# Optimization experiments

Hardware: AMD Instinct MI355X
Metric: run time of the kernel (lower is better)

## Reference

```python
import jax, jax.numpy as jnp
import numpy as np

N_NODES = 50000
N_EDGES = 200000
D = 384
R = 2  # num_relations


def setup_inputs() -> dict:
    key = jax.random.key(0)
    ks = jax.random.split(key, 16)
    inp = {
        "embeddings": jax.random.normal(ks[0], (N_NODES, D), dtype=jnp.float32),
        "edge_index": jax.random.randint(ks[1], (2, N_EDGES), 0, N_NODES, dtype=jnp.int64),
        "edge_type": jax.random.randint(ks[2], (N_EDGES,), 0, R, dtype=jnp.int64),
    }
    # RGCNConv params for 3 layers: per-relation weight, root weight, bias
    s = 1.0 / np.sqrt(D)
    for i, kk in zip((1, 2, 3), range(3)):
        inp[f"W{i}"] = jax.random.uniform(ks[3 + 3 * kk], (R, D, D), dtype=jnp.float32, minval=-s, maxval=s)
        inp[f"root{i}"] = jax.random.uniform(ks[4 + 3 * kk], (D, D), dtype=jnp.float32, minval=-s, maxval=s)
        inp[f"bias{i}"] = jnp.zeros((D,), dtype=jnp.float32)
    return inp


def _rgcn_conv(x, src, dst, edge_type, W, root, bias):
    # PyG RGCNConv with aggr='mean': for each relation, mean-aggregate neighbor
    # features over edges of that relation, then apply relation weight; plus
    # root transform and bias. We transform-then-aggregate (equivalent, linear).
    out = x @ root + bias
    for r in range(R):
        xr = x @ W[r]                                   # [N, D]
        mask = (edge_type == r).astype(x.dtype)         # [E]
        msg = xr[src] * mask[:, None]                   # [E, D] gather
        s = jax.ops.segment_sum(msg, dst, num_segments=N_NODES)    # [N, D]
        cnt = jax.ops.segment_sum(mask, dst, num_segments=N_NODES)  # [N]
        out = out + s / jnp.maximum(cnt, 1.0)[:, None]  # mean (0 if no edges)
    return out


def reference(embeddings, edge_index, edge_type, W1, root1, bias1, W2, root2, bias2, W3, root3, bias3):
    src, dst = edge_index[0], edge_index[1]
    x = jax.nn.relu(_rgcn_conv(embeddings, src, dst, edge_type, W1, root1, bias1))
    # dropout is identity in eval mode
    x = jax.nn.relu(_rgcn_conv(x, src, dst, edge_type, W2, root2, bias2))
    x = _rgcn_conv(x, src, dst, edge_type, W3, root3, bias3)
    return x
```

## Files before the change

### kernel.cpp

```cpp
#include <hip/hip_runtime.h>
#include <hip/hip_bf16.h>


#define D 384
#define KC 1152
#define BM 128
#define BN 128
#define BK 32
#define NKT (KC / BK)
#define NTN (D / BN)

typedef __attribute__((ext_vector_type(8))) short short8;
typedef __attribute__((ext_vector_type(4))) float floatx4;
typedef unsigned int uint;
typedef unsigned short ushort;

#define BAR() asm volatile("s_barrier" ::: "memory")
#define WAIT_VM4() asm volatile("s_waitcnt vmcnt(4)" ::: "memory")
#define WAIT_VM0() asm volatile("s_waitcnt vmcnt(0)" ::: "memory")

__device__ __forceinline__ void load_lds16(const void* g, void* l) {
    __builtin_amdgcn_global_load_lds(
        (const __attribute__((address_space(1))) void*)g,
        (__attribute__((address_space(3))) void*)l, 16, 0, 0);
}

__device__ __forceinline__ ushort f2bf(float x) {
    __hip_bfloat16 h = __float2bfloat16(x);
    return *reinterpret_cast<ushort*>(&h);
}

__device__ __forceinline__ uint pack2(float a, float b) {
    return (uint)f2bf(a) | ((uint)f2bf(b) << 16);
}

__device__ __forceinline__ void stage_rows(const ushort* __restrict__ g,
                                           size_t stride, int koff,
                                           ushort* l, int grow0, int rmax,
                                           int tid)
{
#pragma unroll
    for (int j = 0; j < 2; ++j) {
        const int ch = j * 256 + tid;
        const int row = ch >> 2;
        const int cs = ch & 3;
        const int gc = cs ^ ((row >> 1) & 3);
        const int gr = min(grow0 + row, rmax);
        load_lds16(g + (size_t)gr * stride + koff + gc * 8, l + (size_t)ch * 8);
    }
}

__global__ __launch_bounds__(256, 3) void gemm_fused(
    const ushort* __restrict__ X, const ushort* __restrict__ AG,
    const ushort* __restrict__ BT, const float* __restrict__ bias,
    ushort* __restrict__ Xn, float* __restrict__ outf,
    int M, int nwg, int relu)
{
    __shared__ alignas(16) ushort As[3][BM * BK];
    __shared__ alignas(16) ushort Bs[3][BN * BK];

    const int o = blockIdx.x;
    const int xcd = o & 7, lid = o >> 3;
    const int q = nwg >> 3, r = nwg & 7;
    const int wg = (xcd < r ? xcd * (q + 1) : r * (q + 1) + (xcd - r) * q) + lid;
    const int bnt = wg % NTN, bmt = wg / NTN;
    const int bm = bmt * BM, bn = bnt * BN;

    const int tid = threadIdx.x;
    const int wave = tid >> 6, lane = tid & 63;
    const int wm = wave >> 1;
    const int wn = wave & 1;
    const int l15 = lane & 15, k8 = lane >> 4;

    floatx4 acc[4][4] = {};

    auto stage_a = [&](int kt, ushort* dst) {
        if (kt < 12) stage_rows(X, 384, kt * BK, dst, bm, M - 1, tid);
        else         stage_rows(AG, 768, (kt - 12) * BK, dst, bm, M - 1, tid);
    };

    stage_a(0, As[0]);
    stage_rows(BT, KC, 0, Bs[0], bn, D - 1, tid);
    stage_a(1, As[1]);
    stage_rows(BT, KC, BK, Bs[1], bn, D - 1, tid);
    WAIT_VM4();
    BAR();

    for (int j = 0; j < NKT; ++j) {
        const ushort* Ab = As[j % 3];
        const ushort* Bb = Bs[j % 3];

        short8 af[4], bf[4];
#pragma unroll
        for (int nf = 0; nf < 4; ++nf) {
            const int rr = wn * 64 + nf * 16 + l15;
            af[nf] = *(const short8*)(Bb + rr * BK + ((k8 ^ ((rr >> 1) & 3)) << 3));
        }
#pragma unroll
        for (int mf = 0; mf < 4; ++mf) {
            const int rr = wm * 64 + mf * 16 + l15;
            bf[mf] = *(const short8*)(Ab + rr * BK + ((k8 ^ ((rr >> 1) & 3)) << 3));
        }

        const int js = j + 2;
        if (js < NKT) {
            stage_a(js, As[js % 3]);
            stage_rows(BT, KC, js * BK, Bs[js % 3], bn, D - 1, tid);
        }

        __builtin_amdgcn_s_setprio(1);
#pragma unroll
        for (int nf = 0; nf < 4; ++nf)
#pragma unroll
            for (int mf = 0; mf < 4; ++mf)
                acc[nf][mf] = __builtin_amdgcn_mfma_f32_16x16x32_bf16(
                    af[nf], bf[mf], acc[nf][mf], 0, 0, 0);
        __builtin_amdgcn_s_setprio(0);

        if (j <= NKT - 3)      { WAIT_VM4(); }
        else if (j == NKT - 2) { WAIT_VM0(); }
        BAR();
    }

    const int node0 = bm + wm * 64 + l15;
    const int colg = bn + wn * 64 + k8 * 4;
    float4 bv[4];
#pragma unroll
    for (int nf = 0; nf < 4; ++nf)
        bv[nf] = *(const float4*)(bias + colg + nf * 16);

#pragma unroll
    for (int mf = 0; mf < 4; ++mf) {
        const int node = node0 + mf * 16;
        if (node < M) {
            float v[4][4];
#pragma unroll
            for (int nf = 0; nf < 4; ++nf) {
                v[nf][0] = acc[nf][mf][0] + bv[nf].x;
                v[nf][1] = acc[nf][mf][1] + bv[nf].y;
                v[nf][2] = acc[nf][mf][2] + bv[nf].z;
                v[nf][3] = acc[nf][mf][3] + bv[nf].w;
                if (relu) {
#pragma unroll
                    for (int t = 0; t < 4; ++t) v[nf][t] = fmaxf(v[nf][t], 0.f);
                }
            }
            if (Xn) {
                uint2* rowp = (uint2*)(Xn + (size_t)node * D + colg);
#pragma unroll
                for (int nf = 0; nf < 4; ++nf) {
                    uint2 o2;
                    o2.x = pack2(v[nf][0], v[nf][1]);
                    o2.y = pack2(v[nf][2], v[nf][3]);
                    rowp[nf * 4] = o2;
                }
            } else {
                float4* rowp = (float4*)(outf + (size_t)node * D + colg);
#pragma unroll
                for (int nf = 0; nf < 4; ++nf)
                    rowp[nf * 4] = make_float4(v[nf][0], v[nf][1],
                                               v[nf][2], v[nf][3]);
            }
        }
    }
}


__global__ __launch_bounds__(256) void count_edges(
    const int* __restrict__ dst, const int* __restrict__ et,
    int* __restrict__ cntI, int E, int M)
{
    const int e = blockIdx.x * blockDim.x + threadIdx.x;
    if (e < E) atomicAdd(&cntI[(size_t)et[e] * M + dst[e]], 1);
}

__global__ __launch_bounds__(256) void finalize_cnt(
    const int* __restrict__ cntI, float* __restrict__ invc, int n)
{
    const int i = blockIdx.x * blockDim.x + threadIdx.x;
    if (i < n) invc[i] = 1.0f / (float)max(cntI[i], 1);
}

__global__ __launch_bounds__(1024) void scan_local(
    const int* __restrict__ hist, int* __restrict__ offs,
    int* __restrict__ bsums, int n)
{
    __shared__ int tmp[1024];
    const int tid = threadIdx.x;
    const int i = blockIdx.x * 1024 + tid;
    const int v = (i < n) ? hist[i] : 0;
    tmp[tid] = v;
    __syncthreads();
#pragma unroll
    for (int off = 1; off < 1024; off <<= 1) {
        const int add = (tid >= off) ? tmp[tid - off] : 0;
        __syncthreads();
        tmp[tid] += add;
        __syncthreads();
    }
    if (i < n) offs[i] = tmp[tid] - v;
    if (tid == 1023) bsums[blockIdx.x] = tmp[1023];
}

__global__ __launch_bounds__(1024) void scan_bsums(
    int* __restrict__ bsums, int* __restrict__ total_out, int nb)
{
    __shared__ int tmp[1024];
    const int tid = threadIdx.x;
    const int v = (tid < nb) ? bsums[tid] : 0;
    tmp[tid] = v;
    __syncthreads();
#pragma unroll
    for (int off = 1; off < 1024; off <<= 1) {
        const int add = (tid >= off) ? tmp[tid - off] : 0;
        __syncthreads();
        tmp[tid] += add;
        __syncthreads();
    }
    if (tid < nb) bsums[tid] = tmp[tid] - v;
    if (tid == 1023) *total_out = tmp[1023];
}

__global__ __launch_bounds__(1024) void scan_add(
    int* __restrict__ offs, const int* __restrict__ bsums, int n)
{
    const int i = blockIdx.x * 1024 + threadIdx.x;
    if (i < n) offs[i] += bsums[blockIdx.x];
}

__global__ __launch_bounds__(256) void fill_sorted(
    const int* __restrict__ src, const int* __restrict__ dst,
    const int* __restrict__ et, const int* __restrict__ offs,
    int* __restrict__ cursor, int* __restrict__ sorted, int E, int M)
{
    const int e = blockIdx.x * blockDim.x + threadIdx.x;
    if (e < E) {
        const int key = et[e] * M + dst[e];
        const int pos = offs[key] + atomicAdd(&cursor[key], 1);
        sorted[pos] = src[e];
    }
}

__global__ __launch_bounds__(256) void build_bt(
    const float* __restrict__ root1, const float* __restrict__ W1,
    const float* __restrict__ root2, const float* __restrict__ W2,
    const float* __restrict__ root3, const float* __restrict__ W3,
    ushort* __restrict__ BT)
{
    __shared__ float tile[32][33];
    const int l = blockIdx.z;
    const float* root = (l == 0) ? root1 : (l == 1) ? root2 : root3;
    const float* W    = (l == 0) ? W1    : (l == 1) ? W2    : W3;
    const int k0 = blockIdx.x * 32;
    const int n0 = blockIdx.y * 32;
    const int tx = threadIdx.x & 31;
    const int ty = threadIdx.x >> 5;
    const float* srcm;
    int koff;
    if (k0 < D)          { srcm = root;      koff = 0; }
    else if (k0 < 2 * D) { srcm = W;         koff = D; }
    else                 { srcm = W + D * D; koff = 2 * D; }
#pragma unroll
    for (int i = 0; i < 4; ++i) {
        const int k = k0 - koff + ty + i * 8;
        tile[ty + i * 8][tx] = srcm[(size_t)k * D + n0 + tx];
    }
    __syncthreads();
    ushort* dst = BT + (size_t)l * D * KC;
#pragma unroll
    for (int i = 0; i < 4; ++i) {
        const int nn = n0 + ty + i * 8;
        const int kk = k0 + tx;
        dst[(size_t)nn * KC + kk] = f2bf(tile[tx][ty + i * 8]);
    }
}

__global__ __launch_bounds__(256) void cast_f32_to_bf16(
    const float* __restrict__ x, ushort* __restrict__ y, int n4)
{
    const int i = blockIdx.x * blockDim.x + threadIdx.x;
    if (i < n4) {
        const float4 v = ((const float4*)x)[i];
        uint2 o;
        o.x = pack2(v.x, v.y);
        o.y = pack2(v.z, v.w);
        ((uint2*)y)[i] = o;
    }
}

__global__ __launch_bounds__(256) void aggregate_rel(
    const ushort* __restrict__ X, const int* __restrict__ sorted,
    const int* __restrict__ offs, const float* __restrict__ invc,
    ushort* __restrict__ AG, int M)
{
    const int wave = threadIdx.x >> 6;
    const int lane = threadIdx.x & 63;
    const int d = blockIdx.x * 4 + wave;
    if (d >= M) return;

#pragma unroll
    for (int r = 0; r < 2; ++r) {
        const int key = r * M + d;
        const int beg = offs[key], end = offs[key + 1];
        float g[6] = {0.f, 0.f, 0.f, 0.f, 0.f, 0.f};
        for (int i = beg; i < end; ++i) {
            const int s = sorted[i];
            const uint* tp = (const uint*)(X + (size_t)s * D);
#pragma unroll
            for (int p = 0; p < 3; ++p) {
                const uint b = tp[lane + 64 * p];
                g[2 * p]     += __uint_as_float(b << 16);
                g[2 * p + 1] += __uint_as_float(b & 0xffff0000u);
            }
        }
        const float ic = invc[key];
        uint* op = (uint*)(AG + (size_t)d * (2 * D) + r * D);
#pragma unroll
        for (int p = 0; p < 3; ++p)
            op[lane + 64 * p] = pack2(ic * g[2 * p], ic * g[2 * p + 1]);
    }
}

extern "C" void kernel_launch(void* const* d_in, const int* in_sizes, int n_in,
                              void* d_out, int out_size, void* d_ws, size_t ws_size,
                              hipStream_t stream)
{
    const float* emb   = (const float*)d_in[0];
    const int*   eidx  = (const int*)d_in[1];
    const int*   et    = (const int*)d_in[2];
    const float* W1    = (const float*)d_in[3];
    const float* root1 = (const float*)d_in[4];
    const float* bias1 = (const float*)d_in[5];
    const float* W2    = (const float*)d_in[6];
    const float* root2 = (const float*)d_in[7];
    const float* bias2 = (const float*)d_in[8];
    const float* W3    = (const float*)d_in[9];
    const float* root3 = (const float*)d_in[10];
    const float* bias3 = (const float*)d_in[11];

    float* out = (float*)d_out;
    const int M = in_sizes[0] / D;
    const int E = in_sizes[1] / 2;
    const int* src  = eidx;
    const int* dstv = eidx + E;

    const int n = 2 * M;
    const int nb = (n + 1023) / 1024;

    char* w = (char*)d_ws;
    ushort* Xa  = (ushort*)w;         w += (size_t)M * D * 2;
    ushort* Xb2 = (ushort*)w;         w += (size_t)M * D * 2;
    ushort* AG  = (ushort*)w;         w += (size_t)M * 2 * D * 2;
    ushort* BT  = (ushort*)w;         w += (size_t)3 * D * KC * 2;
    float* invcnt = (float*)w;        w += (size_t)n * 4;
    int* cntI = (int*)w;              w += (size_t)n * 4;
    int* offs = (int*)w;              w += ((size_t)n + 1) * 4;
    int* sorted = (int*)w;            w += (size_t)E * 4;
    int* bsums = (int*)w;

    hipMemsetAsync(cntI, 0, (size_t)n * sizeof(int), stream);
    count_edges<<<(E + 255) / 256, 256, 0, stream>>>(dstv, et, cntI, E, M);
    finalize_cnt<<<(n + 255) / 256, 256, 0, stream>>>(cntI, invcnt, n);
    scan_local<<<nb, 1024, 0, stream>>>(cntI, offs, bsums, n);
    scan_bsums<<<1, 1024, 0, stream>>>(bsums, offs + n, nb);
    scan_add<<<nb, 1024, 0, stream>>>(offs, bsums, n);
    hipMemsetAsync(cntI, 0, (size_t)n * sizeof(int), stream);
    fill_sorted<<<(E + 255) / 256, 256, 0, stream>>>(src, dstv, et, offs, cntI, sorted, E, M);

    build_bt<<<dim3(KC / 32, D / 32, 3), 256, 0, stream>>>(root1, W1, root2, W2, root3, W3, BT);
    cast_f32_to_bf16<<<(M * D / 4 + 255) / 256, 256, 0, stream>>>(emb, Xa, M * D / 4);

    const int Mtiles = (M + BM - 1) / BM;
    const int nwg = Mtiles * NTN;
    const int agg_blocks = (M + 3) / 4;

    aggregate_rel<<<agg_blocks, 256, 0, stream>>>(Xa, sorted, offs, invcnt, AG, M);
    gemm_fused<<<nwg, 256, 0, stream>>>(Xa, AG, BT, bias1, Xb2, nullptr, M, nwg, 1);
    aggregate_rel<<<agg_blocks, 256, 0, stream>>>(Xb2, sorted, offs, invcnt, AG, M);
    gemm_fused<<<nwg, 256, 0, stream>>>(Xb2, AG, BT + (size_t)D * KC, bias2, Xa, nullptr, M, nwg, 1);
    aggregate_rel<<<agg_blocks, 256, 0, stream>>>(Xa, sorted, offs, invcnt, AG, M);
    gemm_fused<<<nwg, 256, 0, stream>>>(Xa, AG, BT + (size_t)2 * D * KC, bias3, nullptr, out, M, nwg, 0);
}
```

Measured before the change: 487.1 us.

## Load weight tiles directly to registers and stage A via registers with double-buffered LDS

```diff
diff --git a/kernel.cpp b/kernel.cpp
--- a/kernel.cpp
+++ b/kernel.cpp
@@ -15,15 +15,7 @@
 typedef unsigned int uint;
 typedef unsigned short ushort;
 
-#define BAR() asm volatile("s_barrier" ::: "memory")
-#define WAIT_VM4() asm volatile("s_waitcnt vmcnt(4)" ::: "memory")
-#define WAIT_VM0() asm volatile("s_waitcnt vmcnt(0)" ::: "memory")
-
-__device__ __forceinline__ void load_lds16(const void* g, void* l) {
-    __builtin_amdgcn_global_load_lds(
-        (const __attribute__((address_space(1))) void*)g,
-        (__attribute__((address_space(3))) void*)l, 16, 0, 0);
-}
+#define LGKM0_BAR() asm volatile("s_waitcnt lgkmcnt(0)\n\ts_barrier" ::: "memory")
 
 __device__ __forceinline__ ushort f2bf(float x) {
     __hip_bfloat16 h = __float2bfloat16(x);
@@ -32,22 +24,6 @@
 
 __device__ __forceinline__ uint pack2(float a, float b) {
     return (uint)f2bf(a) | ((uint)f2bf(b) << 16);
-}
-
-__device__ __forceinline__ void stage_rows(const ushort* __restrict__ g,
-                                           size_t stride, int koff,
-                                           ushort* l, int grow0, int rmax,
-                                           int tid)
-{
-#pragma unroll
-    for (int j = 0; j < 2; ++j) {
-        const int ch = j * 256 + tid;
-        const int row = ch >> 2;
-        const int cs = ch & 3;
-        const int gc = cs ^ ((row >> 1) & 3);
-        const int gr = min(grow0 + row, rmax);
-        load_lds16(g + (size_t)gr * stride + koff + gc * 8, l + (size_t)ch * 8);
-    }
 }
 
 __global__ __launch_bounds__(256, 3) void gemm_fused(
@@ -56,8 +32,8 @@
     ushort* __restrict__ Xn, float* __restrict__ outf,
     int M, int nwg, int relu)
 {
-    __shared__ alignas(16) ushort As[3][BM * BK];
-    __shared__ alignas(16) ushort Bs[3][BN * BK];
+    __shared__ alignas(16) ushort As0[BM * BK];
+    __shared__ alignas(16) ushort As1[BM * BK];
 
     const int o = blockIdx.x;
     const int xcd = o & 7, lid = o >> 3;
@@ -74,52 +50,86 @@
 
     floatx4 acc[4][4] = {};
 
-    auto stage_a = [&](int kt, ushort* dst) {
-        if (kt < 12) stage_rows(X, 384, kt * BK, dst, bm, M - 1, tid);
-        else         stage_rows(AG, 768, (kt - 12) * BK, dst, bm, M - 1, tid);
+    int agr[2], agc[2];
+#pragma unroll
+    for (int jj = 0; jj < 2; ++jj) {
+        const int ch = jj * 256 + tid;
+        const int row = ch >> 2, cs = ch & 3;
+        agc[jj] = cs ^ ((row >> 1) & 3);
+        agr[jj] = min(bm + row, M - 1);
+    }
+
+    auto aglob = [&](int kt, short8* ar) {
+#pragma unroll
+        for (int jj = 0; jj < 2; ++jj) {
+            const ushort* p = (kt < 12)
+                ? X + (size_t)agr[jj] * 384 + kt * BK
+                : AG + (size_t)agr[jj] * 768 + (kt - 12) * BK;
+            ar[jj] = *(const short8*)(p + agc[jj] * 8);
+        }
     };
-
-    stage_a(0, As[0]);
-    stage_rows(BT, KC, 0, Bs[0], bn, D - 1, tid);
-    stage_a(1, As[1]);
-    stage_rows(BT, KC, BK, Bs[1], bn, D - 1, tid);
-    WAIT_VM4();
-    BAR();
-
-    for (int j = 0; j < NKT; ++j) {
-        const ushort* Ab = As[j % 3];
-        const ushort* Bb = Bs[j % 3];
-
-        short8 af[4], bf[4];
+    auto awrite = [&](ushort* Asb, const short8* ar) {
+#pragma unroll
+        for (int jj = 0; jj < 2; ++jj)
+            *(short8*)(Asb + (size_t)(jj * 256 + tid) * 8) = ar[jj];
+    };
+    auto bload = [&](int kt, short8* af) {
 #pragma unroll
         for (int nf = 0; nf < 4; ++nf) {
-            const int rr = wn * 64 + nf * 16 + l15;
-            af[nf] = *(const short8*)(Bb + rr * BK + ((k8 ^ ((rr >> 1) & 3)) << 3));
-        }
+            const int rr = bn + wn * 64 + nf * 16 + l15;
+            af[nf] = *(const short8*)(BT + (size_t)rr * KC + kt * BK + k8 * 8);
+        }
+    };
+    auto aread = [&](const ushort* Asb, short8* bf) {
 #pragma unroll
         for (int mf = 0; mf < 4; ++mf) {
             const int rr = wm * 64 + mf * 16 + l15;
-            bf[mf] = *(const short8*)(Ab + rr * BK + ((k8 ^ ((rr >> 1) & 3)) << 3));
-        }
-
-        const int js = j + 2;
-        if (js < NKT) {
-            stage_a(js, As[js % 3]);
-            stage_rows(BT, KC, js * BK, Bs[js % 3], bn, D - 1, tid);
-        }
-
-        __builtin_amdgcn_s_setprio(1);
-#pragma unroll
-        for (int nf = 0; nf < 4; ++nf)
-#pragma unroll
-            for (int mf = 0; mf < 4; ++mf)
-                acc[nf][mf] = __builtin_amdgcn_mfma_f32_16x16x32_bf16(
-                    af[nf], bf[mf], acc[nf][mf], 0, 0, 0);
-        __builtin_amdgcn_s_setprio(0);
-
-        if (j <= NKT - 3)      { WAIT_VM4(); }
-        else if (j == NKT - 2) { WAIT_VM0(); }
-        BAR();
+            bf[mf] = *(const short8*)(Asb + rr * BK + ((k8 ^ ((rr >> 1) & 3)) << 3));
+        }
+    };
+
+    short8 afA[4], afB[4];
+    short8 arA[2], arB[2];
+
+    aglob(0, arA);
+    bload(0, afA);
+    aglob(1, arB);
+    awrite(As0, arA);
+    LGKM0_BAR();
+
+    for (int j = 0; j < NKT; j += 2) {
+        {
+            short8 bf[4];
+            aread(As0, bf);
+            if (j + 2 < NKT) aglob(j + 2, arA);
+            bload(j + 1, afB);
+            __builtin_amdgcn_s_setprio(1);
+#pragma unroll
+            for (int nf = 0; nf < 4; ++nf)
+#pragma unroll
+                for (int mf = 0; mf < 4; ++mf)
+                    acc[nf][mf] = __builtin_amdgcn_mfma_f32_16x16x32_bf16(
+                        afA[nf], bf[mf], acc[nf][mf], 0, 0, 0);
+            __builtin_amdgcn_s_setprio(0);
+            awrite(As1, arB);
+            LGKM0_BAR();
+        }
+        {
+            short8 bf[4];
+            aread(As1, bf);
+            if (j + 3 < NKT) aglob(j + 3, arB);
+            if (j + 2 < NKT) bload(j + 2, afA);
+            __builtin_amdgcn_s_setprio(1);
+#pragma unroll
+            for (int nf = 0; nf < 4; ++nf)
+#pragma unroll
+                for (int mf = 0; mf < 4; ++mf)
+                    acc[nf][mf] = __builtin_amdgcn_mfma_f32_16x16x32_bf16(
+                        afB[nf], bf[mf], acc[nf][mf], 0, 0, 0);
+            __builtin_amdgcn_s_setprio(0);
+            if (j + 2 < NKT) awrite(As0, arA);
+            LGKM0_BAR();
+        }
     }
 
     const int node0 = bm + wm * 64 + l15;
```

After: 626.1 us. 1.29x slower.

## Parallelize aggregation per (relation,node) wave, batch edge indices, fuse count finalize into scan

Applied to the files above, without the earlier changes.

```diff
diff --git a/kernel.cpp b/kernel.cpp
--- a/kernel.cpp
+++ b/kernel.cpp
@@ -174,21 +174,18 @@
     if (e < E) atomicAdd(&cntI[(size_t)et[e] * M + dst[e]], 1);
 }
 
-__global__ __launch_bounds__(256) void finalize_cnt(
-    const int* __restrict__ cntI, float* __restrict__ invc, int n)
-{
-    const int i = blockIdx.x * blockDim.x + threadIdx.x;
-    if (i < n) invc[i] = 1.0f / (float)max(cntI[i], 1);
-}
-
 __global__ __launch_bounds__(1024) void scan_local(
-    const int* __restrict__ hist, int* __restrict__ offs,
-    int* __restrict__ bsums, int n)
+    int* __restrict__ hist, int* __restrict__ offs,
+    int* __restrict__ bsums, float* __restrict__ invc, int n)
 {
     __shared__ int tmp[1024];
     const int tid = threadIdx.x;
     const int i = blockIdx.x * 1024 + tid;
     const int v = (i < n) ? hist[i] : 0;
+    if (i < n) {
+        invc[i] = 1.0f / (float)max(v, 1);
+        hist[i] = 0;
+    }
     tmp[tid] = v;
     __syncthreads();
 #pragma unroll
@@ -295,30 +292,50 @@
 {
     const int wave = threadIdx.x >> 6;
     const int lane = threadIdx.x & 63;
-    const int d = blockIdx.x * 4 + wave;
-    if (d >= M) return;
-
-#pragma unroll
-    for (int r = 0; r < 2; ++r) {
-        const int key = r * M + d;
-        const int beg = offs[key], end = offs[key + 1];
-        float g[6] = {0.f, 0.f, 0.f, 0.f, 0.f, 0.f};
-        for (int i = beg; i < end; ++i) {
-            const int s = sorted[i];
-            const uint* tp = (const uint*)(X + (size_t)s * D);
-#pragma unroll
-            for (int p = 0; p < 3; ++p) {
-                const uint b = tp[lane + 64 * p];
-                g[2 * p]     += __uint_as_float(b << 16);
-                g[2 * p + 1] += __uint_as_float(b & 0xffff0000u);
-            }
-        }
-        const float ic = invc[key];
-        uint* op = (uint*)(AG + (size_t)d * (2 * D) + r * D);
-#pragma unroll
-        for (int p = 0; p < 3; ++p)
-            op[lane + 64 * p] = pack2(ic * g[2 * p], ic * g[2 * p + 1]);
-    }
+    const int key = blockIdx.x * 4 + wave;
+    if (key >= 2 * M) return;
+    const int r = (key >= M) ? 1 : 0;
+    const int d = key - r * M;
+
+    const int beg = offs[key], end = offs[key + 1];
+    float g0 = 0.f, g1 = 0.f, g2 = 0.f, g3 = 0.f, g4 = 0.f, g5 = 0.f;
+
+    for (int base = beg; base < end; base += 64) {
+        const int cnt = min(end - base, 64);
+        const int idx = (lane < cnt) ? sorted[base + lane] : 0;
+        int e = 0;
+        for (; e + 2 <= cnt; e += 2) {
+            const int s0 = __shfl(idx, e);
+            const int s1 = __shfl(idx, e + 1);
+            const uint* t0 = (const uint*)(X + (size_t)s0 * D);
+            const uint* t1 = (const uint*)(X + (size_t)s1 * D);
+            const uint a0 = t0[lane], a1 = t0[lane + 64], a2 = t0[lane + 128];
+            const uint b0 = t1[lane], b1 = t1[lane + 64], b2 = t1[lane + 128];
+            g0 += __uint_as_float(a0 << 16) + __uint_as_float(b0 << 16);
+            g1 += __uint_as_float(a0 & 0xffff0000u) + __uint_as_float(b0 & 0xffff0000u);
+            g2 += __uint_as_float(a1 << 16) + __uint_as_float(b1 << 16);
+            g3 += __uint_as_float(a1 & 0xffff0000u) + __uint_as_float(b1 & 0xffff0000u);
+            g4 += __uint_as_float(a2 << 16) + __uint_as_float(b2 << 16);
+            g5 += __uint_as_float(a2 & 0xffff0000u) + __uint_as_float(b2 & 0xffff0000u);
+        }
+        if (e < cnt) {
+            const int s0 = __shfl(idx, e);
+            const uint* t0 = (const uint*)(X + (size_t)s0 * D);
+            const uint a0 = t0[lane], a1 = t0[lane + 64], a2 = t0[lane + 128];
+            g0 += __uint_as_float(a0 << 16);
+            g1 += __uint_as_float(a0 & 0xffff0000u);
+            g2 += __uint_as_float(a1 << 16);
+            g3 += __uint_as_float(a1 & 0xffff0000u);
+            g4 += __uint_as_float(a2 << 16);
+            g5 += __uint_as_float(a2 & 0xffff0000u);
+        }
+    }
+
+    const float ic = invc[key];
+    uint* op = (uint*)(AG + (size_t)d * (2 * D) + r * D);
+    op[lane]       = pack2(ic * g0, ic * g1);
+    op[lane + 64]  = pack2(ic * g2, ic * g3);
+    op[lane + 128] = pack2(ic * g4, ic * g5);
 }
 
 extern "C" void kernel_launch(void* const* d_in, const int* in_sizes, int n_in,
@@ -360,11 +377,9 @@
 
     hipMemsetAsync(cntI, 0, (size_t)n * sizeof(int), stream);
     count_edges<<<(E + 255) / 256, 256, 0, stream>>>(dstv, et, cntI, E, M);
-    finalize_cnt<<<(n + 255) / 256, 256, 0, stream>>>(cntI, invcnt, n);
-    scan_local<<<nb, 1024, 0, stream>>>(cntI, offs, bsums, n);
+    scan_local<<<nb, 1024, 0, stream>>>(cntI, offs, bsums, invcnt, n);
     scan_bsums<<<1, 1024, 0, stream>>>(bsums, offs + n, nb);
     scan_add<<<nb, 1024, 0, stream>>>(offs, bsums, n);
-    hipMemsetAsync(cntI, 0, (size_t)n * sizeof(int), stream);
     fill_sorted<<<(E + 255) / 256, 256, 0, stream>>>(src, dstv, et, offs, cntI, sorted, E, M);
 
     build_bt<<<dim3(KC / 32, D / 32, 3), 256, 0, stream>>>(root1, W1, root2, W2, root3, W3, BT);
@@ -372,7 +387,7 @@
 
     const int Mtiles = (M + BM - 1) / BM;
     const int nwg = Mtiles * NTN;
-    const int agg_blocks = (M + 3) / 4;
+    const int agg_blocks = (2 * M + 3) / 4;
 
     aggregate_rel<<<agg_blocks, 256, 0, stream>>>(Xa, sorted, offs, invcnt, AG, M);
     gemm_fused<<<nwg, 256, 0, stream>>>(Xa, AG, BT, bias1, Xb2, nullptr, M, nwg, 1);
```

Result: faster. 472.8 us (-2.9%).
